# Optimization experiments

Hardware: AMD Instinct MI355X
Metric: run time of the kernel (lower is better)

## Reference

```python
import jax, jax.numpy as jnp
import numpy as np


def setup_inputs() -> dict:
    key = jax.random.key(0)
    k1, k2 = jax.random.split(key)
    b, c, h, w = 16, 512, 64, 64
    rgb_feat = jax.random.normal(k1, (b, c, h, w), dtype=jnp.float32)
    depth_feat = jax.random.normal(k2, (b, c, h, w), dtype=jnp.float32)
    return {"rgb_feat": rgb_feat, "depth_feat": depth_feat}


def reference(rgb_feat, depth_feat):
    b, c, h, w = rgb_feat.shape
    rgb_r = rgb_feat.reshape(b, c, h * w)      # (b, c, hw)
    depth_r = depth_feat.reshape(b, c, h * w)  # (b, c, hw)
    # interaction: (b, c, c) = depth_r @ rgb_r^T
    interaction = jnp.einsum('bcs,bds->bcd', depth_r, rgb_r)
    interaction = jax.nn.sigmoid(interaction)
    # depth_weighted: (b, c, hw) = interaction @ depth_r
    depth_weighted = jnp.einsum('bcd,bds->bcs', interaction, depth_r)
    fused = rgb_feat + depth_weighted.reshape(b, c, h, w)
    return fused
```

## Files before the change

kernel.cpp:

```cpp
#include <hip/hip_runtime.h>

#define B_ 16
#define C_ 512
#define S_ 4096

typedef __attribute__((ext_vector_type(4))) float float4v;
typedef __attribute__((ext_vector_type(8))) short short8;
typedef __attribute__((ext_vector_type(4))) short short4v;

typedef __attribute__((address_space(1))) unsigned int as1_uint;
typedef __attribute__((address_space(3))) unsigned int as3_uint;

#define ASYNC16(gsrc, ldst) \
  __builtin_amdgcn_global_load_lds((as1_uint*)(gsrc), (as3_uint*)(ldst), 16, 0, 0)

__device__ __forceinline__ unsigned short f2bf(float f) {
  unsigned u = __builtin_bit_cast(unsigned, f);
  u = u + 0x7FFFu + ((u >> 16) & 1u);
  return (unsigned short)(u >> 16);
}

__global__ __launch_bounds__(256) void k_transpose(
    const float* __restrict__ depth, unsigned short* __restrict__ depthT) {
  __shared__ float tile[32][33];
  int b = blockIdx.z;
  int s0 = blockIdx.x * 32, d0 = blockIdx.y * 32;
  int tx = threadIdx.x & 31, ty = threadIdx.x >> 5;
  const float* src = depth + (b * C_ + d0) * S_ + s0;
#pragma unroll
  for (int p = 0; p < 4; ++p) {
    int d = ty + p * 8;
    tile[d][tx] = src[d * S_ + tx];
  }
  __syncthreads();
  unsigned short* dst = depthT + (b * S_ + s0) * C_ + d0;
#pragma unroll
  for (int p = 0; p < 4; ++p) {
    int s = ty + p * 8;
    dst[s * C_ + tx] = f2bf(tile[tx][s]);
  }
}

__global__ __launch_bounds__(256) void k_gemm1(
    const float* __restrict__ depth, const float* __restrict__ rgb,
    unsigned short* __restrict__ I) {
  const int BK = 32, LDA = 40;
  __shared__ __align__(16) short As[128 * LDA];
  __shared__ __align__(16) short Bs[128 * LDA];
  int b = blockIdx.z;
  int c0 = blockIdx.x * 128, d0 = blockIdx.y * 128;
  int t = threadIdx.x;
  const float* Abase = depth + (b * C_ + c0) * S_;
  const float* Bbase = rgb + (b * C_ + d0) * S_;
  int w = t >> 6, l = t & 63, half = l >> 4, r = l & 15;
  int wm = (w >> 1) * 64, wn = (w & 1) * 64;

  float4v acc[4][4] = {};
  float4v pa[4], pb[4];

#pragma unroll
  for (int q = 0; q < 4; ++q) {
    int idx = q * 256 + t, row = idx >> 3, ch = idx & 7;
    pa[q] = *(const float4v*)(Abase + row * S_ + ch * 4);
    pb[q] = *(const float4v*)(Bbase + row * S_ + ch * 4);
  }

  for (int kt = 0; kt < S_ / BK; ++kt) {
#pragma unroll
    for (int q = 0; q < 4; ++q) {
      int idx = q * 256 + t, row = idx >> 3, ch = idx & 7;
      short4v sa = {(short)f2bf(pa[q].x), (short)f2bf(pa[q].y),
                    (short)f2bf(pa[q].z), (short)f2bf(pa[q].w)};
      short4v sb = {(short)f2bf(pb[q].x), (short)f2bf(pb[q].y),
                    (short)f2bf(pb[q].z), (short)f2bf(pb[q].w)};
      *(short4v*)&As[row * LDA + ch * 4] = sa;
      *(short4v*)&Bs[row * LDA + ch * 4] = sb;
    }
    __syncthreads();
    if (kt + 1 < S_ / BK) {
      int k0 = (kt + 1) * BK;
#pragma unroll
      for (int q = 0; q < 4; ++q) {
        int idx = q * 256 + t, row = idx >> 3, ch = idx & 7;
        pa[q] = *(const float4v*)(Abase + row * S_ + k0 + ch * 4);
        pb[q] = *(const float4v*)(Bbase + row * S_ + k0 + ch * 4);
      }
    }
    short8 af[4], bfr[4];
#pragma unroll
    for (int i = 0; i < 4; ++i)
      af[i] = *(const short8*)&As[(wm + 16 * i + r) * LDA + half * 8];
#pragma unroll
    for (int j = 0; j < 4; ++j)
      bfr[j] = *(const short8*)&Bs[(wn + 16 * j + r) * LDA + half * 8];
#pragma unroll
    for (int i = 0; i < 4; ++i)
#pragma unroll
      for (int j = 0; j < 4; ++j)
        acc[i][j] =
            __builtin_amdgcn_mfma_f32_16x16x32_bf16(af[i], bfr[j], acc[i][j], 0, 0, 0);
    __syncthreads();
  }

#pragma unroll
  for (int i = 0; i < 4; ++i)
#pragma unroll
    for (int j = 0; j < 4; ++j)
#pragma unroll
      for (int reg = 0; reg < 4; ++reg) {
        int c = c0 + wm + 16 * i + half * 4 + reg;
        int d = d0 + wn + 16 * j + r;
        float x = acc[i][j][reg];
        float sg = 1.0f / (1.0f + __expf(-x));
        I[(b * C_ + c) * C_ + d] = f2bf(sg);
      }
}

__global__ __launch_bounds__(256) void k_gemm2(
    const unsigned short* __restrict__ I, const unsigned short* __restrict__ depthT,
    const float* __restrict__ rgb, float* __restrict__ out) {
  const int BK = 32;
  __shared__ __align__(16) short As[128 * BK];
  __shared__ __align__(16) short Bs[128 * BK];
  int b = blockIdx.z;
  int c0 = blockIdx.x * 128, s0 = blockIdx.y * 128;
  int t = threadIdx.x;
  const unsigned short* Ab = I + (b * C_ + c0) * C_;
  const unsigned short* Bb = depthT + (b * S_ + s0) * C_;
  int w = t >> 6, l = t & 63, half = l >> 4, r = l & 15;
  int wm = (w >> 1) * 64, wn = (w & 1) * 64;
  float4v acc[4][4] = {};

  for (int k0 = 0; k0 < C_; k0 += BK) {
    __syncthreads();
#pragma unroll
    for (int q = 0; q < 2; ++q) {
      int idx = q * 256 + t;
      ASYNC16(Ab + (idx >> 2) * C_ + k0 + (idx & 3) * 8, &As[idx * 8]);
    }
#pragma unroll
    for (int q = 0; q < 2; ++q) {
      int idx = q * 256 + t;
      ASYNC16(Bb + (idx >> 2) * C_ + k0 + (idx & 3) * 8, &Bs[idx * 8]);
    }
    __syncthreads();

    short8 af[4], bfr[4];
#pragma unroll
    for (int i = 0; i < 4; ++i)
      af[i] = *(const short8*)&As[(wm + 16 * i + r) * BK + half * 8];
#pragma unroll
    for (int j = 0; j < 4; ++j)
      bfr[j] = *(const short8*)&Bs[(wn + 16 * j + r) * BK + half * 8];
#pragma unroll
    for (int i = 0; i < 4; ++i)
#pragma unroll
      for (int j = 0; j < 4; ++j)
        acc[i][j] =
            __builtin_amdgcn_mfma_f32_16x16x32_bf16(af[i], bfr[j], acc[i][j], 0, 0, 0);
  }

#pragma unroll
  for (int i = 0; i < 4; ++i)
#pragma unroll
    for (int j = 0; j < 4; ++j)
#pragma unroll
      for (int reg = 0; reg < 4; ++reg) {
        int c = c0 + wm + 16 * i + half * 4 + reg;
        int s = s0 + wn + 16 * j + r;
        int o = (b * C_ + c) * S_ + s;
        out[o] = rgb[o] + acc[i][j][reg];
      }
}

extern "C" void kernel_launch(void* const* d_in, const int* in_sizes, int n_in,
                              void* d_out, int out_size, void* d_ws, size_t ws_size,
                              hipStream_t stream) {
  const float* rgb = (const float*)d_in[0];
  const float* depth = (const float*)d_in[1];
  float* out = (float*)d_out;
  unsigned short* depthT = (unsigned short*)d_ws;
  unsigned short* I = (unsigned short*)((char*)d_ws + (size_t)B_ * S_ * C_ * 2);

  k_transpose<<<dim3(S_ / 32, C_ / 32, B_), 256, 0, stream>>>(depth, depthT);
  k_gemm1<<<dim3(C_ / 128, C_ / 128, B_), 256, 0, stream>>>(depth, rgb, I);
  k_gemm2<<<dim3(C_ / 128, S_ / 128, B_), 256, 0, stream>>>(I, depthT, rgb, out);
}
```

Baseline: 528.3 us.

## Split-K the first GEMM with separate reduce-sigmoid kernel and vectorize transpose

Splits the K=4096 reduction of the first GEMM into four slices so four times as many blocks run, writing fp32 partials into the output buffer as scratch. A new kernel sums the partials and applies sigmoid and bf16 conversion. The transpose kernel is rewritten with a larger tile, float4 loads and packed short4 stores. This adds 64MB of partial traffic and an extra launch in exchange for better CU occupancy on the first GEMM.

```diff
diff --git a/kernel.cpp b/kernel.cpp
--- a/kernel.cpp
+++ b/kernel.cpp
@@ -22,36 +22,48 @@
 
 __global__ __launch_bounds__(256) void k_transpose(
     const float* __restrict__ depth, unsigned short* __restrict__ depthT) {
-  __shared__ float tile[32][33];
+  __shared__ float tile[64][129];
   int b = blockIdx.z;
-  int s0 = blockIdx.x * 32, d0 = blockIdx.y * 32;
-  int tx = threadIdx.x & 31, ty = threadIdx.x >> 5;
+  int s0 = blockIdx.x * 64, d0 = blockIdx.y * 128;
+  int t = threadIdx.x;
   const float* src = depth + (b * C_ + d0) * S_ + s0;
 #pragma unroll
-  for (int p = 0; p < 4; ++p) {
-    int d = ty + p * 8;
-    tile[d][tx] = src[d * S_ + tx];
+  for (int it = 0; it < 8; ++it) {
+    int slot = it * 256 + t;
+    int d = slot >> 4, l16 = slot & 15;
+    float4v v = *(const float4v*)(src + d * S_ + l16 * 4);
+    tile[l16 * 4 + 0][d] = v.x;
+    tile[l16 * 4 + 1][d] = v.y;
+    tile[l16 * 4 + 2][d] = v.z;
+    tile[l16 * 4 + 3][d] = v.w;
   }
   __syncthreads();
   unsigned short* dst = depthT + (b * S_ + s0) * C_ + d0;
 #pragma unroll
-  for (int p = 0; p < 4; ++p) {
-    int s = ty + p * 8;
-    dst[s * C_ + tx] = f2bf(tile[tx][s]);
+  for (int it = 0; it < 8; ++it) {
+    int slot = it * 256 + t;
+    int s = slot >> 5, l32 = slot & 31;
+    float x0 = tile[s][l32 * 4 + 0];
+    float x1 = tile[s][l32 * 4 + 1];
+    float x2 = tile[s][l32 * 4 + 2];
+    float x3 = tile[s][l32 * 4 + 3];
+    short4v o = {(short)f2bf(x0), (short)f2bf(x1), (short)f2bf(x2), (short)f2bf(x3)};
+    *(short4v*)(dst + s * C_ + l32 * 4) = o;
   }
 }
 
 __global__ __launch_bounds__(256) void k_gemm1(
     const float* __restrict__ depth, const float* __restrict__ rgb,
-    unsigned short* __restrict__ I) {
+    float* __restrict__ partial) {
   const int BK = 32, LDA = 40;
   __shared__ __align__(16) short As[128 * LDA];
   __shared__ __align__(16) short Bs[128 * LDA];
-  int b = blockIdx.z;
+  int bz = blockIdx.z;
+  int b = bz >> 2, ks = bz & 3;
   int c0 = blockIdx.x * 128, d0 = blockIdx.y * 128;
   int t = threadIdx.x;
-  const float* Abase = depth + (b * C_ + c0) * S_;
-  const float* Bbase = rgb + (b * C_ + d0) * S_;
+  const float* Abase = depth + (size_t)(b * C_ + c0) * S_ + ks * 1024;
+  const float* Bbase = rgb + (size_t)(b * C_ + d0) * S_ + ks * 1024;
   int w = t >> 6, l = t & 63, half = l >> 4, r = l & 15;
   int wm = (w >> 1) * 64, wn = (w & 1) * 64;
 
@@ -65,7 +77,8 @@
     pb[q] = *(const float4v*)(Bbase + row * S_ + ch * 4);
   }
 
-  for (int kt = 0; kt < S_ / BK; ++kt) {
+  const int NKT = 1024 / BK;
+  for (int kt = 0; kt < NKT; ++kt) {
 #pragma unroll
     for (int q = 0; q < 4; ++q) {
       int idx = q * 256 + t, row = idx >> 3, ch = idx & 7;
@@ -77,7 +90,7 @@
       *(short4v*)&Bs[row * LDA + ch * 4] = sb;
     }
     __syncthreads();
-    if (kt + 1 < S_ / BK) {
+    if (kt + 1 < NKT) {
       int k0 = (kt + 1) * BK;
 #pragma unroll
       for (int q = 0; q < 4; ++q) {
@@ -102,6 +115,7 @@
     __syncthreads();
   }
 
+  float* P = partial + ((size_t)(ks * B_ + b) * C_) * C_;
 #pragma unroll
   for (int i = 0; i < 4; ++i)
 #pragma unroll
@@ -110,10 +124,24 @@
       for (int reg = 0; reg < 4; ++reg) {
         int c = c0 + wm + 16 * i + half * 4 + reg;
         int d = d0 + wn + 16 * j + r;
-        float x = acc[i][j][reg];
-        float sg = 1.0f / (1.0f + __expf(-x));
-        I[(b * C_ + c) * C_ + d] = f2bf(sg);
+        P[(size_t)c * C_ + d] = acc[i][j][reg];
       }
+}
+
+__global__ __launch_bounds__(256) void k_reduce(const float* __restrict__ p,
+                                                unsigned short* __restrict__ I) {
+  const size_t n = (size_t)B_ * C_ * C_;
+  size_t idx = ((size_t)blockIdx.x * 256 + threadIdx.x) * 4;
+  float4v s = *(const float4v*)(p + idx);
+  s += *(const float4v*)(p + n + idx);
+  s += *(const float4v*)(p + 2 * n + idx);
+  s += *(const float4v*)(p + 3 * n + idx);
+  float g0 = 1.0f / (1.0f + __expf(-s.x));
+  float g1 = 1.0f / (1.0f + __expf(-s.y));
+  float g2 = 1.0f / (1.0f + __expf(-s.z));
+  float g3 = 1.0f / (1.0f + __expf(-s.w));
+  short4v o = {(short)f2bf(g0), (short)f2bf(g1), (short)f2bf(g2), (short)f2bf(g3)};
+  *(short4v*)(I + idx) = o;
 }
 
 __global__ __launch_bounds__(256) void k_gemm2(
@@ -125,8 +153,8 @@
   int b = blockIdx.z;
   int c0 = blockIdx.x * 128, s0 = blockIdx.y * 128;
   int t = threadIdx.x;
-  const unsigned short* Ab = I + (b * C_ + c0) * C_;
-  const unsigned short* Bb = depthT + (b * S_ + s0) * C_;
+  const unsigned short* Ab = I + (size_t)(b * C_ + c0) * C_;
+  const unsigned short* Bb = depthT + (size_t)(b * S_ + s0) * C_;
   int w = t >> 6, l = t & 63, half = l >> 4, r = l & 15;
   int wm = (w >> 1) * 64, wn = (w & 1) * 64;
   float4v acc[4][4] = {};
@@ -168,7 +196,7 @@
       for (int reg = 0; reg < 4; ++reg) {
         int c = c0 + wm + 16 * i + half * 4 + reg;
         int s = s0 + wn + 16 * j + r;
-        int o = (b * C_ + c) * S_ + s;
+        size_t o = (size_t)(b * C_ + c) * S_ + s;
         out[o] = rgb[o] + acc[i][j][reg];
       }
 }
@@ -181,8 +209,10 @@
   float* out = (float*)d_out;
   unsigned short* depthT = (unsigned short*)d_ws;
   unsigned short* I = (unsigned short*)((char*)d_ws + (size_t)B_ * S_ * C_ * 2);
-
-  k_transpose<<<dim3(S_ / 32, C_ / 32, B_), 256, 0, stream>>>(depth, depthT);
-  k_gemm1<<<dim3(C_ / 128, C_ / 128, B_), 256, 0, stream>>>(depth, rgb, I);
+  float* partial = out;
+
+  k_transpose<<<dim3(S_ / 64, C_ / 128, B_), 256, 0, stream>>>(depth, depthT);
+  k_gemm1<<<dim3(C_ / 128, C_ / 128, B_ * 4), 256, 0, stream>>>(depth, rgb, partial);
+  k_reduce<<<dim3((B_ * C_ * C_) / 1024), 256, 0, stream>>>(partial, I);
   k_gemm2<<<dim3(C_ / 128, S_ / 128, B_), 256, 0, stream>>>(I, depthT, rgb, out);
 }
```

Result: faster. 492.8 us (-6.7%).
